# Kernel optimization log

Hardware: AMD Instinct MI355X
Metric: run time of the kernel (lower is better)

The kernel has to match this reference:

```python
import jax, jax.numpy as jnp
import numpy as np

B, N, C, H = 2, 2048, 1024, 16
D = C // H
SCALE = D ** -0.5


def setup_inputs() -> dict:
    key = jax.random.key(0)
    ks = jax.random.split(key, 4)
    s = 0.02
    return {
        "x": jax.random.normal(ks[0], (B, N, C), dtype=jnp.float32),
        "f": jax.random.normal(ks[1], (B, N, C), dtype=jnp.float32),
        "W_qkv": jax.random.normal(ks[2], (C, 3 * C), dtype=jnp.float32) * s,
        "W_proj": jax.random.normal(ks[3], (C, C), dtype=jnp.float32) * s,
        "b_proj": jnp.zeros((C,), dtype=jnp.float32),
    }


def reference(x, f, W_qkv, W_proj, b_proj):
    b, n, c = x.shape
    h, d = H, c // H
    # qkv projection -> (B,N,3,H,D) -> q,k,v each (B,H,N,D)
    qkv = (x @ W_qkv).reshape(b, n, 3, h, d)
    q = jnp.transpose(qkv[:, :, 0], (0, 2, 1, 3))
    k = jnp.transpose(qkv[:, :, 1], (0, 2, 1, 3))
    v = jnp.transpose(qkv[:, :, 2], (0, 2, 1, 3))
    # full NxN scores, faithful to the original manual MHA
    attn = jax.nn.softmax(jnp.einsum("bhqd,bhkd->bhqk", q, k) * SCALE, axis=-1)
    av = jnp.einsum("bhqk,bhkd->bhqd", attn, v)  # (B,H,N,D)
    # pre-residual output branch
    attn2gcn = jnp.transpose(av, (0, 2, 1, 3)).reshape(b, n, c)
    # residual fuse with f (reshaped per-head in torch; equivalent to flat add)
    fused = attn2gcn + f
    out = fused @ W_proj + b_proj
    return (out, attn2gcn)
```

## Files before the change

kernel.cpp:

```cpp
#include <hip/hip_runtime.h>
#include <hip/hip_bf16.h>

#define OUT1_OFF 4194304
#define QSCALE 0.1803368801111204f

typedef __attribute__((ext_vector_type(8))) short bf16x8;
typedef __attribute__((ext_vector_type(4))) float f32x4;

__device__ __forceinline__ unsigned short f2bf(float x) {
    unsigned u = __float_as_uint(x);
    u += 0x7FFFu + ((u >> 16) & 1u);
    return (unsigned short)(u >> 16);
}

__device__ __forceinline__ void gl2lds16(const unsigned short* g, unsigned short* l) {
    __builtin_amdgcn_global_load_lds(
        (const __attribute__((address_space(1))) unsigned int*)g,
        (__attribute__((address_space(3))) unsigned int*)l, 16, 0, 0);
}

__global__ __launch_bounds__(256) void prep(const float* __restrict__ x,
                                            const float* __restrict__ Wqkv,
                                            const float* __restrict__ Wproj,
                                            unsigned short* __restrict__ xb,
                                            unsigned short* __restrict__ wqkvT,
                                            unsigned short* __restrict__ wprojT) {
    __shared__ float T[64][65];
    const int bid = blockIdx.x, tid = threadIdx.x;
    if (bid < 4096) {
        int i = bid * 256 + tid;
        float4 v = reinterpret_cast<const float4*>(x)[i];
        ushort4 o = make_ushort4(f2bf(v.x), f2bf(v.y), f2bf(v.z), f2bf(v.w));
        reinterpret_cast<ushort4*>(xb)[i] = o;
        return;
    }
    const float* in; unsigned short* out; int Nd, bx, by;
    if (bid < 4864) { int t = bid - 4096; in = Wqkv;  out = wqkvT;  Nd = 3072; bx = t % 48; by = t / 48; }
    else            { int t = bid - 4864; in = Wproj; out = wprojT; Nd = 1024; bx = t % 16; by = t / 16; }
    const int Kd = 1024;
    const int r0 = by * 64, c0 = bx * 64;
    const int tr = tid >> 3, tc = (tid & 7) * 8;
#pragma unroll
    for (int rr = 0; rr < 64; rr += 32) {
        const float4* p = reinterpret_cast<const float4*>(&in[(r0 + tr + rr) * Nd + c0 + tc]);
        float4 v0 = p[0], v1 = p[1];
        T[tr + rr][tc + 0] = v0.x; T[tr + rr][tc + 1] = v0.y;
        T[tr + rr][tc + 2] = v0.z; T[tr + rr][tc + 3] = v0.w;
        T[tr + rr][tc + 4] = v1.x; T[tr + rr][tc + 5] = v1.y;
        T[tr + rr][tc + 6] = v1.z; T[tr + rr][tc + 7] = v1.w;
    }
    __syncthreads();
#pragma unroll
    for (int rr = 0; rr < 64; rr += 32) {
        int orow = tr + rr;
        ushort4 o0 = make_ushort4(f2bf(T[tc + 0][orow]), f2bf(T[tc + 1][orow]),
                                  f2bf(T[tc + 2][orow]), f2bf(T[tc + 3][orow]));
        ushort4 o1 = make_ushort4(f2bf(T[tc + 4][orow]), f2bf(T[tc + 5][orow]),
                                  f2bf(T[tc + 6][orow]), f2bf(T[tc + 7][orow]));
        unsigned short* dst = &out[(c0 + orow) * Kd + r0 + tc];
        *reinterpret_cast<ushort4*>(dst) = o0;
        *reinterpret_cast<ushort4*>(dst + 4) = o1;
    }
}

__global__ __launch_bounds__(256) void gemm_qkv(const unsigned short* __restrict__ A,
                                                const unsigned short* __restrict__ Bt,
                                                unsigned short* __restrict__ qb,
                                                unsigned short* __restrict__ kb,
                                                unsigned short* __restrict__ vtb) {
    __shared__ __align__(16) unsigned short Sh[18432];
    unsigned short* As = Sh;
    unsigned short* Bs = Sh + 8192;
    const int tid = threadIdx.x;
    const int w = tid >> 6, lane = tid & 63, quad = lane >> 4, l15 = lane & 15;
    const int m0 = blockIdx.y * 128, n0 = blockIdx.x * 128;
    const int wm = (w & 1) * 64, wn = (w >> 1) * 64;
    const int nbase = n0 + wn;
    const int t = nbase >> 10;
    const bool qk = (t < 2);
    const int sw = (l15 & 7) << 3;
    f32x4 acc[4][4] = {};
    for (int k0 = 0; k0 < 1024; k0 += 64) {
        __syncthreads();
#pragma unroll
        for (int tt = 0; tt < 4; ++tt) {
            int c = tt * 256 + tid;
            int row = c >> 3, jg = ((c & 7) ^ (row & 7)) * 8;
            gl2lds16(&A[(m0 + row) * 1024 + k0 + jg], &As[c * 8]);
            gl2lds16(&Bt[(n0 + row) * 1024 + k0 + jg], &Bs[c * 8]);
        }
        __syncthreads();
#pragma unroll
        for (int kk = 0; kk < 2; ++kk) {
            bf16x8 af[4], bfr[4];
#pragma unroll
            for (int i = 0; i < 4; ++i)
                af[i] = *reinterpret_cast<const bf16x8*>(
                    &As[(wm + i * 16 + l15) * 64 + ((((kk * 4 + quad) << 3) ^ sw))]);
#pragma unroll
            for (int j = 0; j < 4; ++j)
                bfr[j] = *reinterpret_cast<const bf16x8*>(
                    &Bs[(wn + j * 16 + l15) * 64 + ((((kk * 4 + quad) << 3) ^ sw))]);
            if (qk) {
#pragma unroll
                for (int i = 0; i < 4; ++i)
#pragma unroll
                    for (int j = 0; j < 4; ++j)
                        acc[i][j] = __builtin_amdgcn_mfma_f32_16x16x32_bf16(bfr[j], af[i], acc[i][j], 0, 0, 0);
            } else {
#pragma unroll
                for (int i = 0; i < 4; ++i)
#pragma unroll
                    for (int j = 0; j < 4; ++j)
                        acc[i][j] = __builtin_amdgcn_mfma_f32_16x16x32_bf16(af[i], bfr[j], acc[i][j], 0, 0, 0);
            }
        }
    }
    __syncthreads();
    unsigned short* scr = Sh + w * 4608;
    const int mb = m0 + wm;
    const int b = mb >> 11;
    const int h = (nbase & 1023) >> 6;
    const float sc = (t == 0) ? QSCALE : 1.f;
    if (qk) {
#pragma unroll
        for (int i = 0; i < 4; ++i) {
            int row = i * 16 + l15;
#pragma unroll
            for (int j = 0; j < 4; ++j) {
                unsigned short h0 = f2bf(acc[i][j][0] * sc), h1 = f2bf(acc[i][j][1] * sc);
                unsigned short h2 = f2bf(acc[i][j][2] * sc), h3 = f2bf(acc[i][j][3] * sc);
                uint2 pk = make_uint2((unsigned)h0 | ((unsigned)h1 << 16),
                                      (unsigned)h2 | ((unsigned)h3 << 16));
                *reinterpret_cast<uint2*>(&scr[row * 72 + j * 16 + quad * 4]) = pk;
            }
        }
        asm volatile("s_waitcnt lgkmcnt(0)" ::: "memory");
        unsigned short* dst = (t == 0 ? qb : kb) + (((b * 16 + h) * 2048) + (mb & 2047)) * 64;
#pragma unroll
        for (int p = 0; p < 8; ++p) {
            int idx = p * 64 + lane;
            *reinterpret_cast<uint4*>(&dst[idx * 8]) =
                *reinterpret_cast<const uint4*>(&scr[(idx >> 3) * 72 + (idx & 7) * 8]);
        }
    } else {
        const int kblk = (mb & 2047) >> 6;
#pragma unroll
        for (int i = 0; i < 4; ++i) {
            int slot0 = ((i & 2) << 4) | (quad << 3) | ((i & 1) << 2);
#pragma unroll
            for (int j = 0; j < 4; ++j) {
                unsigned short h0 = f2bf(acc[i][j][0]), h1 = f2bf(acc[i][j][1]);
                unsigned short h2 = f2bf(acc[i][j][2]), h3 = f2bf(acc[i][j][3]);
                uint2 pk = make_uint2((unsigned)h0 | ((unsigned)h1 << 16),
                                      (unsigned)h2 | ((unsigned)h3 << 16));
                *reinterpret_cast<uint2*>(&scr[(j * 16 + l15) * 72 + slot0]) = pk;
            }
        }
        asm volatile("s_waitcnt lgkmcnt(0)" ::: "memory");
        unsigned short* vtile = vtb + (((b * 16 + h) * 32) + kblk) * 4096;
#pragma unroll
        for (int p = 0; p < 8; ++p) {
            int idx = p * 64 + lane;
            *reinterpret_cast<uint4*>(&vtile[idx * 8]) =
                *reinterpret_cast<const uint4*>(&scr[(idx >> 3) * 72 + (idx & 7) * 8]);
        }
    }
}

__global__ __launch_bounds__(512, 4) void attn_kernel(const unsigned short* __restrict__ qb,
                                                      const unsigned short* __restrict__ kb,
                                                      const unsigned short* __restrict__ vtb,
                                                      const float* __restrict__ f,
                                                      float* __restrict__ attn2_out,
                                                      unsigned short* __restrict__ fusedb) {
    __shared__ __align__(16) unsigned char SMEM[69632];
    unsigned short* S16 = reinterpret_cast<unsigned short*>(SMEM);
    const int tid = threadIdx.x;
    const int w = tid >> 6, lane = tid & 63, quad = lane >> 4, l15 = lane & 15;
    const int qg = w & 3, kh = w >> 2;
    const int bh = blockIdx.x;
    const int q0w = blockIdx.y * 128 + qg * 32;
    const unsigned short* qr = &qb[(bh * 2048 + q0w + l15) * 64 + quad * 8];
    bf16x8 ql0 = *reinterpret_cast<const bf16x8*>(qr);
    bf16x8 ql1 = *reinterpret_cast<const bf16x8*>(qr + 32);
    bf16x8 ql2 = *reinterpret_cast<const bf16x8*>(qr + 1024);
    bf16x8 ql3 = *reinterpret_cast<const bf16x8*>(qr + 1056);
    const unsigned short* kt0 = kb + bh * 131072;
    const unsigned short* vt0 = vtb + bh * 131072;
    const int gu = (((tid & ~7) | ((tid & 7) ^ ((tid >> 3) & 7))) << 3);
    const int sw = (l15 & 7) << 3;
    f32x4 O0[4] = {}, O1[4] = {};
    f32x4 asum0 = {}, asum1 = {};
    bf16x8 ones;
#pragma unroll
    for (int j = 0; j < 8; ++j) ones[j] = (short)0x3F80;

#define STAGE(IT, BUF) do { unsigned short* db_ = &S16[(BUF) * 16384 + tid * 8]; \
        const int go_ = (IT) * 4096 + gu;                                        \
        gl2lds16(kt0 + go_, db_);                                                \
        gl2lds16(vt0 + go_, db_ + 4096);                                         \
        gl2lds16(kt0 + 65536 + go_, db_ + 8192);                                 \
        gl2lds16(vt0 + 65536 + go_, db_ + 12288); } while (0)

    auto body = [&](int buf) {
        const unsigned short* Kb = &S16[buf * 16384 + kh * 8192];
        const unsigned short* Vb = Kb + 4096;
        f32x4 Ta[4], Tb[4];
        __builtin_amdgcn_s_setprio(1);
#pragma unroll
        for (int s = 0; s < 4; ++s) {
            const unsigned short* kr = &Kb[(s * 16 + l15) * 64];
            bf16x8 k0 = *reinterpret_cast<const bf16x8*>(&kr[(quad << 3) ^ sw]);
            bf16x8 k1 = *reinterpret_cast<const bf16x8*>(&kr[((quad + 4) << 3) ^ sw]);
            f32x4 za = {}, zb = {};
            za = __builtin_amdgcn_mfma_f32_16x16x32_bf16(k0, ql0, za, 0, 0, 0);
            za = __builtin_amdgcn_mfma_f32_16x16x32_bf16(k1, ql1, za, 0, 0, 0);
            zb = __builtin_amdgcn_mfma_f32_16x16x32_bf16(k0, ql2, zb, 0, 0, 0);
            zb = __builtin_amdgcn_mfma_f32_16x16x32_bf16(k1, ql3, zb, 0, 0, 0);
            Ta[s] = za; Tb[s] = zb;
        }
        __builtin_amdgcn_s_setprio(0);
        float pa_[4][4], pb_[4][4];
#pragma unroll
        for (int s = 0; s < 4; ++s)
#pragma unroll
            for (int r = 0; r < 4; ++r) {
                pa_[s][r] = __builtin_amdgcn_exp2f(Ta[s][r]);
                pb_[s][r] = __builtin_amdgcn_exp2f(Tb[s][r]);
            }
        uint4 u0, u1, v0u, v1u;
        u0.x = __builtin_amdgcn_perm(__float_as_uint(pa_[0][1]), __float_as_uint(pa_[0][0]), 0x07060302u);
        u0.y = __builtin_amdgcn_perm(__float_as_uint(pa_[0][3]), __float_as_uint(pa_[0][2]), 0x07060302u);
        u0.z = __builtin_amdgcn_perm(__float_as_uint(pa_[1][1]), __float_as_uint(pa_[1][0]), 0x07060302u);
        u0.w = __builtin_amdgcn_perm(__float_as_uint(pa_[1][3]), __float_as_uint(pa_[1][2]), 0x07060302u);
        u1.x = __builtin_amdgcn_perm(__float_as_uint(pa_[2][1]), __float_as_uint(pa_[2][0]), 0x07060302u);
        u1.y = __builtin_amdgcn_perm(__float_as_uint(pa_[2][3]), __float_as_uint(pa_[2][2]), 0x07060302u);
        u1.z = __builtin_amdgcn_perm(__float_as_uint(pa_[3][1]), __float_as_uint(pa_[3][0]), 0x07060302u);
        u1.w = __builtin_amdgcn_perm(__float_as_uint(pa_[3][3]), __float_as_uint(pa_[3][2]), 0x07060302u);
        v0u.x = __builtin_amdgcn_perm(__float_as_uint(pb_[0][1]), __float_as_uint(pb_[0][0]), 0x07060302u);
        v0u.y = __builtin_amdgcn_perm(__float_as_uint(pb_[0][3]), __float_as_uint(pb_[0][2]), 0x07060302u);
        v0u.z = __builtin_amdgcn_perm(__float_as_uint(pb_[1][1]), __float_as_uint(pb_[1][0]), 0x07060302u);
        v0u.w = __builtin_amdgcn_perm(__float_as_uint(pb_[1][3]), __float_as_uint(pb_[1][2]), 0x07060302u);
        v1u.x = __builtin_amdgcn_perm(__float_as_uint(pb_[2][1]), __float_as_uint(pb_[2][0]), 0x07060302u);
        v1u.y = __builtin_amdgcn_perm(__float_as_uint(pb_[2][3]), __float_as_uint(pb_[2][2]), 0x07060302u);
        v1u.z = __builtin_amdgcn_perm(__float_as_uint(pb_[3][1]), __float_as_uint(pb_[3][0]), 0x07060302u);
        v1u.w = __builtin_amdgcn_perm(__float_as_uint(pb_[3][3]), __float_as_uint(pb_[3][2]), 0x07060302u);
        bf16x8 paa0 = __builtin_bit_cast(bf16x8, u0);
        bf16x8 paa1 = __builtin_bit_cast(bf16x8, u1);
        bf16x8 pba0 = __builtin_bit_cast(bf16x8, v0u);
        bf16x8 pba1 = __builtin_bit_cast(bf16x8, v1u);
        asum0 = __builtin_amdgcn_mfma_f32_16x16x32_bf16(paa0, ones, asum0, 0, 0, 0);
        asum0 = __builtin_amdgcn_mfma_f32_16x16x32_bf16(paa1, ones, asum0, 0, 0, 0);
        asum1 = __builtin_amdgcn_mfma_f32_16x16x32_bf16(pba0, ones, asum1, 0, 0, 0);
        asum1 = __builtin_amdgcn_mfma_f32_16x16x32_bf16(pba1, ones, asum1, 0, 0, 0);
        __builtin_amdgcn_s_setprio(1);
#pragma unroll
        for (int c4 = 0; c4 < 4; ++c4) {
            const unsigned short* vr = &Vb[(c4 * 16 + l15) * 64];
            bf16x8 v0 = *reinterpret_cast<const bf16x8*>(&vr[(quad << 3) ^ sw]);
            bf16x8 v1 = *reinterpret_cast<const bf16x8*>(&vr[((quad + 4) << 3) ^ sw]);
            O0[c4] = __builtin_amdgcn_mfma_f32_16x16x32_bf16(paa0, v0, O0[c4], 0, 0, 0);
            O0[c4] = __builtin_amdgcn_mfma_f32_16x16x32_bf16(paa1, v1, O0[c4], 0, 0, 0);
            O1[c4] = __builtin_amdgcn_mfma_f32_16x16x32_bf16(pba0, v0, O1[c4], 0, 0, 0);
            O1[c4] = __builtin_amdgcn_mfma_f32_16x16x32_bf16(pba1, v1, O1[c4], 0, 0, 0);
        }
        __builtin_amdgcn_s_setprio(0);
    };

    STAGE(0, 0);
    for (int it = 0; it < 16; it += 2) {
        __syncthreads();
        STAGE(it + 1, 1);
        body(0);
        __syncthreads();
        if (it + 2 < 16) STAGE(it + 2, 0);
        body(1);
    }
#undef STAGE

    __syncthreads();
    float* scr = reinterpret_cast<float*>(SMEM);
    {
        float* myr = scr + w * 2176;
#pragma unroll
        for (int c4 = 0; c4 < 4; ++c4) {
            int dcol = c4 * 16 + l15;
#pragma unroll
            for (int r = 0; r < 4; ++r) {
                myr[(quad * 4 + r) * 68 + dcol] = O0[c4][r];
                myr[(16 + quad * 4 + r) * 68 + dcol] = O1[c4][r];
            }
        }
        if (l15 == 0) {
#pragma unroll
            for (int r = 0; r < 4; ++r) {
                myr[(quad * 4 + r) * 68 + 64] = asum0[r];
                myr[(16 + quad * 4 + r) * 68 + 64] = asum1[r];
            }
        }
    }
    __syncthreads();
    const int b = bh >> 4, h = bh & 15;
    const float* rA = scr + qg * 2176;
    const float* rB = rA + 4 * 2176;
    const int row = kh * 16 + (lane >> 2);
    const int dq = (lane & 3) * 16;
    const int base = (b * 2048 + (q0w + row)) * 1024 + h * 64;
    const float den = rA[row * 68 + 64] + rB[row * 68 + 64];
    const float inv = 1.f / den;
#pragma unroll
    for (int j = 0; j < 4; ++j) {
        int d = dq + j * 4;
        f32x4 pa = *reinterpret_cast<const f32x4*>(&rA[row * 68 + d]);
        f32x4 pb = *reinterpret_cast<const f32x4*>(&rB[row * 68 + d]);
        float4 fv = *reinterpret_cast<const float4*>(&f[base + d]);
        float o0 = (pa[0] + pb[0]) * inv;
        float o1 = (pa[1] + pb[1]) * inv;
        float o2 = (pa[2] + pb[2]) * inv;
        float o3 = (pa[3] + pb[3]) * inv;
        *reinterpret_cast<float4*>(&attn2_out[base + d]) = make_float4(o0, o1, o2, o3);
        ushort4 pk = make_ushort4(f2bf(o0 + fv.x), f2bf(o1 + fv.y),
                                  f2bf(o2 + fv.z), f2bf(o3 + fv.w));
        *reinterpret_cast<ushort4*>(&fusedb[base + d]) = pk;
    }
}

__global__ __launch_bounds__(256) void gemm_proj(const unsigned short* __restrict__ A,
                                                 const unsigned short* __restrict__ Bt,
                                                 const float* __restrict__ bias,
                                                 float* __restrict__ out) {
    __shared__ __align__(16) unsigned short As[8192];
    __shared__ __align__(16) unsigned short Bs[4096];
    const int tid = threadIdx.x;
    const int w = tid >> 6, lane = tid & 63, quad = lane >> 4, l15 = lane & 15;
    const int m0 = blockIdx.y * 128, n0 = blockIdx.x * 64;
    const int wm = (w & 1) * 64, wn = (w >> 1) * 32;
    const int sw = (l15 & 7) << 3;
    f32x4 acc[4][2] = {};
    for (int k0 = 0; k0 < 1024; k0 += 64) {
        __syncthreads();
#pragma unroll
        for (int t = 0; t < 4; ++t) {
            int c = t * 256 + tid;
            int row = c >> 3, jg = ((c & 7) ^ (row & 7)) * 8;
            gl2lds16(&A[(m0 + row) * 1024 + k0 + jg], &As[c * 8]);
            if (t < 2) gl2lds16(&Bt[(n0 + row) * 1024 + k0 + jg], &Bs[c * 8]);
        }
        __syncthreads();
#pragma unroll
        for (int kk = 0; kk < 2; ++kk) {
            bf16x8 af[4], bfr[2];
#pragma unroll
            for (int i = 0; i < 4; ++i)
                af[i] = *reinterpret_cast<const bf16x8*>(
                    &As[(wm + i * 16 + l15) * 64 + ((((kk * 4 + quad) << 3) ^ sw))]);
#pragma unroll
            for (int j = 0; j < 2; ++j)
                bfr[j] = *reinterpret_cast<const bf16x8*>(
                    &Bs[(wn + j * 16 + l15) * 64 + ((((kk * 4 + quad) << 3) ^ sw))]);
#pragma unroll
            for (int i = 0; i < 4; ++i)
#pragma unroll
                for (int j = 0; j < 2; ++j)
                    acc[i][j] = __builtin_amdgcn_mfma_f32_16x16x32_bf16(af[i], bfr[j], acc[i][j], 0, 0, 0);
        }
    }
#pragma unroll
    for (int j = 0; j < 2; ++j) {
        int n = n0 + wn + j * 16 + l15;
        float bv = bias[n];
#pragma unroll
        for (int i = 0; i < 4; ++i)
#pragma unroll
            for (int r = 0; r < 4; ++r) {
                int m = m0 + wm + i * 16 + quad * 4 + r;
                out[m * 1024 + n] = acc[i][j][r] + bv;
            }
    }
}

extern "C" void kernel_launch(void* const* d_in, const int* in_sizes, int n_in,
                              void* d_out, int out_size, void* d_ws, size_t ws_size,
                              hipStream_t stream) {
    const float* x      = (const float*)d_in[0];
    const float* f      = (const float*)d_in[1];
    const float* W_qkv  = (const float*)d_in[2];
    const float* W_proj = (const float*)d_in[3];
    const float* b_proj = (const float*)d_in[4];
    float* out   = (float*)d_out;
    float* attn2 = out + OUT1_OFF;

    char* ws = (char*)d_ws;
    unsigned short* xb     = (unsigned short*)(ws);
    unsigned short* wqkvT  = (unsigned short*)(ws + 8388608);
    unsigned short* wprojT = (unsigned short*)(ws + 14680064);
    unsigned short* qb     = (unsigned short*)(ws + 16777216);
    unsigned short* kb     = (unsigned short*)(ws + 25165824);
    unsigned short* vtb    = (unsigned short*)(ws + 33554432);
    unsigned short* fusedb = (unsigned short*)(ws + 41943040);

    prep<<<5120, 256, 0, stream>>>(x, W_qkv, W_proj, xb, wqkvT, wprojT);
    gemm_qkv<<<dim3(24, 32), 256, 0, stream>>>(xb, wqkvT, qb, kb, vtb);
    attn_kernel<<<dim3(32, 16), 512, 0, stream>>>(qb, kb, vtb, f, attn2, fusedb);
    gemm_proj<<<dim3(16, 32), 256, 0, stream>>>(fusedb, wprojT, b_proj, out);
}
```

Before: 187.0 us.

## Double-buffer LDS tiles in QKV and projection GEMMs to overlap loads with MFMA

Both GEMM kernels now hold two LDS tile buffers. The next K-slice is issued through global_load_lds while MFMAs consume the current buffer, and the main loop is unrolled by two so it alternates buffers. The goal is to hide global-memory latency behind compute instead of stalling at a barrier every K step. In exchange, the QKV kernel grows to 64KB of LDS and the projection kernel to 48KB, which can lower occupancy. The compiler may also insert conservative vmcnt waits before LDS reads, which would limit the overlap.

```diff
diff --git a/kernel.cpp b/kernel.cpp
--- a/kernel.cpp
+++ b/kernel.cpp
@@ -68,9 +68,7 @@
                                                 unsigned short* __restrict__ qb,
                                                 unsigned short* __restrict__ kb,
                                                 unsigned short* __restrict__ vtb) {
-    __shared__ __align__(16) unsigned short Sh[18432];
-    unsigned short* As = Sh;
-    unsigned short* Bs = Sh + 8192;
+    __shared__ __align__(16) unsigned short Sh[32768];
     const int tid = threadIdx.x;
     const int w = tid >> 6, lane = tid & 63, quad = lane >> 4, l15 = lane & 15;
     const int m0 = blockIdx.y * 128, n0 = blockIdx.x * 128;
@@ -80,27 +78,32 @@
     const bool qk = (t < 2);
     const int sw = (l15 & 7) << 3;
     f32x4 acc[4][4] = {};
-    for (int k0 = 0; k0 < 1024; k0 += 64) {
-        __syncthreads();
-#pragma unroll
-        for (int tt = 0; tt < 4; ++tt) {
-            int c = tt * 256 + tid;
-            int row = c >> 3, jg = ((c & 7) ^ (row & 7)) * 8;
-            gl2lds16(&A[(m0 + row) * 1024 + k0 + jg], &As[c * 8]);
-            gl2lds16(&Bt[(n0 + row) * 1024 + k0 + jg], &Bs[c * 8]);
-        }
-        __syncthreads();
+
+#define QKV_STAGE(K0, BUF) do {                                               \
+        unsigned short* As_ = &Sh[(BUF) * 16384];                             \
+        unsigned short* Bs_ = As_ + 8192;                                     \
+        _Pragma("unroll")                                                     \
+        for (int tt = 0; tt < 4; ++tt) {                                      \
+            int c = tt * 256 + tid;                                           \
+            int row = c >> 3, jg = ((c & 7) ^ (row & 7)) * 8;                 \
+            gl2lds16(&A[(m0 + row) * 1024 + (K0) + jg], &As_[c * 8]);         \
+            gl2lds16(&Bt[(n0 + row) * 1024 + (K0) + jg], &Bs_[c * 8]);        \
+        } } while (0)
+
+    auto compute = [&](int buf) {
+        const unsigned short* As_ = &Sh[buf * 16384];
+        const unsigned short* Bs_ = As_ + 8192;
 #pragma unroll
         for (int kk = 0; kk < 2; ++kk) {
             bf16x8 af[4], bfr[4];
 #pragma unroll
             for (int i = 0; i < 4; ++i)
                 af[i] = *reinterpret_cast<const bf16x8*>(
-                    &As[(wm + i * 16 + l15) * 64 + ((((kk * 4 + quad) << 3) ^ sw))]);
+                    &As_[(wm + i * 16 + l15) * 64 + ((((kk * 4 + quad) << 3) ^ sw))]);
 #pragma unroll
             for (int j = 0; j < 4; ++j)
                 bfr[j] = *reinterpret_cast<const bf16x8*>(
-                    &Bs[(wn + j * 16 + l15) * 64 + ((((kk * 4 + quad) << 3) ^ sw))]);
+                    &Bs_[(wn + j * 16 + l15) * 64 + ((((kk * 4 + quad) << 3) ^ sw))]);
             if (qk) {
 #pragma unroll
                 for (int i = 0; i < 4; ++i)
@@ -115,7 +118,18 @@
                         acc[i][j] = __builtin_amdgcn_mfma_f32_16x16x32_bf16(af[i], bfr[j], acc[i][j], 0, 0, 0);
             }
         }
-    }
+    };
+
+    QKV_STAGE(0, 0);
+    for (int k0 = 0; k0 < 1024; k0 += 128) {
+        __syncthreads();
+        QKV_STAGE(k0 + 64, 1);
+        compute(0);
+        __syncthreads();
+        if (k0 + 128 < 1024) QKV_STAGE(k0 + 128, 0);
+        compute(1);
+    }
+#undef QKV_STAGE
     __syncthreads();
     unsigned short* scr = Sh + w * 4608;
     const int mb = m0 + wm;
@@ -330,42 +344,58 @@
                                                  const unsigned short* __restrict__ Bt,
                                                  const float* __restrict__ bias,
                                                  float* __restrict__ out) {
-    __shared__ __align__(16) unsigned short As[8192];
-    __shared__ __align__(16) unsigned short Bs[4096];
+    __shared__ __align__(16) unsigned short Sh[24576];
     const int tid = threadIdx.x;
     const int w = tid >> 6, lane = tid & 63, quad = lane >> 4, l15 = lane & 15;
     const int m0 = blockIdx.y * 128, n0 = blockIdx.x * 64;
     const int wm = (w & 1) * 64, wn = (w >> 1) * 32;
     const int sw = (l15 & 7) << 3;
     f32x4 acc[4][2] = {};
-    for (int k0 = 0; k0 < 1024; k0 += 64) {
-        __syncthreads();
-#pragma unroll
-        for (int t = 0; t < 4; ++t) {
-            int c = t * 256 + tid;
-            int row = c >> 3, jg = ((c & 7) ^ (row & 7)) * 8;
-            gl2lds16(&A[(m0 + row) * 1024 + k0 + jg], &As[c * 8]);
-            if (t < 2) gl2lds16(&Bt[(n0 + row) * 1024 + k0 + jg], &Bs[c * 8]);
-        }
-        __syncthreads();
+
+#define PROJ_STAGE(K0, BUF) do {                                              \
+        unsigned short* As_ = &Sh[(BUF) * 12288];                             \
+        unsigned short* Bs_ = As_ + 8192;                                     \
+        _Pragma("unroll")                                                     \
+        for (int tt = 0; tt < 4; ++tt) {                                      \
+            int c = tt * 256 + tid;                                           \
+            int row = c >> 3, jg = ((c & 7) ^ (row & 7)) * 8;                 \
+            gl2lds16(&A[(m0 + row) * 1024 + (K0) + jg], &As_[c * 8]);         \
+            if (tt < 2) gl2lds16(&Bt[(n0 + row) * 1024 + (K0) + jg], &Bs_[c * 8]); \
+        } } while (0)
+
+    auto compute = [&](int buf) {
+        const unsigned short* As_ = &Sh[buf * 12288];
+        const unsigned short* Bs_ = As_ + 8192;
 #pragma unroll
         for (int kk = 0; kk < 2; ++kk) {
             bf16x8 af[4], bfr[2];
 #pragma unroll
             for (int i = 0; i < 4; ++i)
                 af[i] = *reinterpret_cast<const bf16x8*>(
-                    &As[(wm + i * 16 + l15) * 64 + ((((kk * 4 + quad) << 3) ^ sw))]);
+                    &As_[(wm + i * 16 + l15) * 64 + ((((kk * 4 + quad) << 3) ^ sw))]);
 #pragma unroll
             for (int j = 0; j < 2; ++j)
                 bfr[j] = *reinterpret_cast<const bf16x8*>(
-                    &Bs[(wn + j * 16 + l15) * 64 + ((((kk * 4 + quad) << 3) ^ sw))]);
+                    &Bs_[(wn + j * 16 + l15) * 64 + ((((kk * 4 + quad) << 3) ^ sw))]);
 #pragma unroll
             for (int i = 0; i < 4; ++i)
 #pragma unroll
                 for (int j = 0; j < 2; ++j)
                     acc[i][j] = __builtin_amdgcn_mfma_f32_16x16x32_bf16(af[i], bfr[j], acc[i][j], 0, 0, 0);
         }
-    }
+    };
+
+    PROJ_STAGE(0, 0);
+    for (int k0 = 0; k0 < 1024; k0 += 128) {
+        __syncthreads();
+        PROJ_STAGE(k0 + 64, 1);
+        compute(0);
+        __syncthreads();
+        if (k0 + 128 < 1024) PROJ_STAGE(k0 + 128, 0);
+        compute(1);
+    }
+#undef PROJ_STAGE
+
 #pragma unroll
     for (int j = 0; j < 2; ++j) {
         int n = n0 + wn + j * 16 + l15;
```

Result: faster. 176.2 us, median of 2 (-5.8%).
